# Kernel tuning notes

Measured on AMD Instinct MI355X. Metric: run time of the kernel, lower is better.

## Reference

```python
import jax, jax.numpy as jnp
import numpy as np

N_NODES = 100000
N_EDGES = 1600000
N_GRAPHS = 256
D = 128
L = 3
N_OUT = 10


def setup_inputs() -> dict:
    key = jax.random.key(0)
    ks = jax.random.split(key, 6)
    x = jax.random.normal(ks[0], (N_NODES, D), dtype=jnp.float32)
    edge_index = jax.random.randint(ks[1], (2, N_EDGES), 0, N_NODES, dtype=jnp.int64)
    batch = jnp.sort(jax.random.randint(ks[2], (N_NODES,), 0, N_GRAPHS, dtype=jnp.int64))
    conv_w = jax.random.normal(ks[3], (L, D, D), dtype=jnp.float32) * (1.0 / np.sqrt(D))
    conv_b = jnp.zeros((L, D), dtype=jnp.float32)
    out_w = jax.random.normal(ks[4], (3 * D, N_OUT), dtype=jnp.float32) * (1.0 / np.sqrt(3 * D))
    out_b = jnp.zeros((N_OUT,), dtype=jnp.float32)
    return {"x": x, "edge_index": edge_index, "batch": batch,
            "conv_w": conv_w, "conv_b": conv_b, "out_w": out_w, "out_b": out_b}


def reference(x, edge_index, batch, conv_w, conv_b, out_w, out_b):
    N = x.shape[0]
    # --- add self-loops (PyG GCNConv default) ---
    loop = jnp.arange(N, dtype=edge_index.dtype)
    src = jnp.concatenate([edge_index[0], loop])  # [E+N]
    dst = jnp.concatenate([edge_index[1], loop])
    # --- symmetric normalization: deg computed on dst (col) ---
    deg = jax.ops.segment_sum(jnp.ones_like(dst, dtype=x.dtype), dst, num_segments=N)
    dinv = jnp.where(deg > 0, jax.lax.rsqrt(jnp.maximum(deg, 1.0)), 0.0)
    norm = dinv[src] * dinv[dst]  # [E+N]

    h = x
    for l in range(conv_w.shape[0]):
        h = h @ conv_w[l]                                   # [N, D] transform first
        msg = h[src] * norm[:, None]                        # gather + scale
        h = jax.ops.segment_sum(msg, dst, num_segments=N)   # scatter-add
        h = jax.nn.relu(h + conv_b[l])

    # --- global max / mean / add pooling over graphs ---
    B = N_GRAPHS
    gmax = jax.ops.segment_max(h, batch, num_segments=B)
    gsum = jax.ops.segment_sum(h, batch, num_segments=B)
    cnt = jax.ops.segment_sum(jnp.ones((N, 1), h.dtype), batch, num_segments=B)
    gmean = gsum / jnp.maximum(cnt, 1.0)
    pooled = jnp.concatenate([gmax, gmean, gsum], axis=1)   # [B, 3D]
    # dropout p=0.5 is identity in eval mode
    return pooled @ out_w + out_b
```

## Files before the change

### kernel.cpp

```cpp
#include <hip/hip_runtime.h>
#include <hip/hip_bf16.h>

#define D 128
#define NP 8
#define DPB 64
#define KPB (DPB * NP)
#define SUB 64
#define CAP_SUB 64

typedef __attribute__((ext_vector_type(8))) __bf16 bf16x8;
typedef __attribute__((ext_vector_type(4))) float f32x4;
typedef __attribute__((ext_vector_type(4))) short s16x4;
typedef __attribute__((ext_vector_type(8))) short s16x8;

static __device__ __forceinline__ short f2bf(float f) {
    union { float f; unsigned u; } in; in.f = f;
    unsigned u = in.u;
    u += 0x7fffu + ((u >> 16) & 1u);
    return (short)(u >> 16);
}

__global__ void k_bucket(const int* __restrict__ src, const int* __restrict__ dst,
                         int* __restrict__ bcnt, int* __restrict__ staging,
                         int E, int KBE) {
    int i = blockIdx.x * 256 + threadIdx.x;
    if (i >= E) return;
    int d = dst[i], s = src[i];
    int b = d >> 6;
    int key = ((d & 63) << 3) | (s >> 14);
    int j = blockIdx.x & (SUB - 1);
    int slot = atomicAdd(&bcnt[j * KBE + b], 1);
    if (slot < CAP_SUB) staging[((size_t)j * KBE + b) * CAP_SUB + slot] = (key << 17) | s;
}

__global__ void k_btot(const int* __restrict__ bcnt, int* __restrict__ btot, int KBE) {
    int b = blockIdx.x * 256 + threadIdx.x;
    if (b >= KBE) return;
    int v = 0;
    #pragma unroll
    for (int j = 0; j < SUB; j++) {
        int c = bcnt[j * KBE + b];
        v += (c > CAP_SUB) ? CAP_SUB : c;
    }
    btot[b] = v;
}

__global__ void k_bscan(const int* __restrict__ btot, int* __restrict__ bbase,
                        int* __restrict__ row_ptr, int nkeys, int KBE) {
    __shared__ int sm[512];
    __shared__ int carry;
    int t = threadIdx.x;
    if (t == 0) carry = 0;
    __syncthreads();
    for (int c0 = 0; c0 < KBE; c0 += 512) {
        int b = c0 + t;
        int v = (b < KBE) ? btot[b] : 0;
        sm[t] = v;
        __syncthreads();
        for (int off = 1; off < 512; off <<= 1) {
            int x = (t >= off) ? sm[t - off] : 0;
            __syncthreads();
            sm[t] += x;
            __syncthreads();
        }
        if (b < KBE) bbase[b] = sm[t] - v + carry;
        __syncthreads();
        if (t == 0) carry += sm[511];
        __syncthreads();
    }
    if (t == 0) { bbase[KBE] = carry; row_ptr[nkeys] = carry; }
}

__global__ __launch_bounds__(256) void k_build(
    const int* __restrict__ staging, const int* __restrict__ bcnt,
    const int* __restrict__ bbase, int* __restrict__ row_ptr,
    int* __restrict__ csr_src, float* __restrict__ dinv, int N, int KBE)
{
    const int b = blockIdx.x;
    const int tid = threadIdx.x;
    __shared__ int cnt[KPB];
    __shared__ int subn[SUB];
    __shared__ int chunkbuf[256];
    __shared__ int carry;

    if (tid < SUB) {
        int c = bcnt[tid * KBE + b];
        subn[tid] = (c > CAP_SUB) ? CAP_SUB : c;
    }
    for (int k = tid; k < KPB; k += 256) cnt[k] = 0;
    if (tid == 0) carry = 0;
    __syncthreads();

    const int base = bbase[b];
    const int nb = bbase[b + 1] - base;
    const int j = tid >> 2, l4 = tid & 3;
    const int* __restrict__ sreg = staging + ((size_t)j * KBE + b) * CAP_SUB;
    const int sn = subn[j];

    for (int e = l4; e < sn; e += 4)
        atomicAdd(&cnt[sreg[e] >> 17], 1);
    __syncthreads();

    #pragma unroll 1
    for (int c = 0; c < KPB / 256; c++) {
        int idx = c * 256 + tid;
        int v = cnt[idx];
        chunkbuf[tid] = v;
        __syncthreads();
        for (int off = 1; off < 256; off <<= 1) {
            int x = (tid >= off) ? chunkbuf[tid - off] : 0;
            __syncthreads();
            chunkbuf[tid] += x;
            __syncthreads();
        }
        cnt[idx] = chunkbuf[tid] - v + carry;
        __syncthreads();
        if (tid == 255) carry += chunkbuf[255];
        __syncthreads();
    }

    for (int k = tid; k < KPB; k += 256)
        row_ptr[(size_t)b * KPB + k] = base + cnt[k];
    for (int dl = tid; dl < DPB; dl += 256) {
        int d = b * DPB + dl;
        if (d < N) {
            int hi2 = (dl == DPB - 1) ? nb : cnt[(dl + 1) * NP];
            int deg = hi2 - cnt[dl * NP];
            dinv[d] = rsqrtf((float)deg + 1.0f);
        }
    }
    __syncthreads();

    for (int e = l4; e < sn; e += 4) {
        int w = sreg[e];
        int slot = base + atomicAdd(&cnt[w >> 17], 1);
        csr_src[slot] = w & 0x1FFFF;
    }
}

__global__ void k_gseg(const int* __restrict__ batch, int* __restrict__ gstart,
                       int* __restrict__ gcnt, int N, int B) {
    int g = blockIdx.x * blockDim.x + threadIdx.x;
    if (g > B) return;
    int lo = 0, hi = N;
    while (lo < hi) {
        int mid = (lo + hi) >> 1;
        if (batch[mid] < g) lo = mid + 1; else hi = mid;
    }
    gstart[g] = lo;
    if (g < B) {
        int lo2 = lo, hi2 = N;
        while (lo2 < hi2) {
            int mid = (lo2 + hi2) >> 1;
            if (batch[mid] < g + 1) lo2 = mid + 1; else hi2 = mid;
        }
        gcnt[g] = lo2 - lo;
    }
}

__global__ void k_cvt_x(const float* __restrict__ x, const float* __restrict__ dinv,
                        short* __restrict__ xb, int total4) {
    int i = blockIdx.x * blockDim.x + threadIdx.x;
    if (i < total4) {
        float d = dinv[i >> 5];
        float4 v = ((const float4*)x)[i];
        s16x4 o;
        o.x = f2bf(v.x * d); o.y = f2bf(v.y * d);
        o.z = f2bf(v.z * d); o.w = f2bf(v.w * d);
        ((s16x4*)xb)[i] = o;
    }
}

__global__ void k_cvt_w(const float* __restrict__ W, short* __restrict__ Wt, int total) {
    int i = blockIdx.x * blockDim.x + threadIdx.x;
    if (i < total) {
        int l = i >> 14;
        int rem = i & 16383;
        int n = rem >> 7;
        int k = rem & 127;
        Wt[i] = f2bf(W[(l << 14) + (k << 7) + n]);
    }
}

__global__ __launch_bounds__(256) void k_layer(
    const short* __restrict__ hin, const int* __restrict__ row_ptr,
    const int* __restrict__ csr_src, const float* __restrict__ dinv,
    const short* __restrict__ Wt, const float* __restrict__ bias,
    short* __restrict__ hout, float* __restrict__ hrelu, int N, int mode)
{
    __shared__ __align__(16) short tile[16 * 128];
    const int tid = threadIdx.x;
    const int wave = tid >> 6;
    const int lane = tid & 63;
    const int group = lane >> 4;
    const int lg = lane & 15;
    const int off = lg * 8;
    const int node_base = blockIdx.x * 16;
    const int r = wave * 4 + group;
    const int i = node_base + r;

    short* dstp = &tile[r * 128 + ((lg ^ (r & 7)) << 3)];
    if (i < N) {
        float acc[8];
        bf16x8 v = *(const bf16x8*)(hin + (size_t)i * D + off);
        #pragma unroll
        for (int k = 0; k < 8; k++) acc[k] = (float)v[k];

        int t = row_ptr[i * NP];
        const int end = row_ptr[i * NP + NP];
        for (; t + 4 <= end; t += 4) {
            int i0 = csr_src[t + 0], i1 = csr_src[t + 1];
            int i2 = csr_src[t + 2], i3 = csr_src[t + 3];
            bf16x8 v0 = *(const bf16x8*)(hin + (size_t)i0 * D + off);
            bf16x8 v1 = *(const bf16x8*)(hin + (size_t)i1 * D + off);
            bf16x8 v2 = *(const bf16x8*)(hin + (size_t)i2 * D + off);
            bf16x8 v3 = *(const bf16x8*)(hin + (size_t)i3 * D + off);
            #pragma unroll
            for (int k = 0; k < 8; k++)
                acc[k] += (((float)v0[k] + (float)v1[k]) + ((float)v2[k] + (float)v3[k]));
        }
        for (; t < end; t++) {
            int i0 = csr_src[t];
            bf16x8 v0 = *(const bf16x8*)(hin + (size_t)i0 * D + off);
            #pragma unroll
            for (int k = 0; k < 8; k++) acc[k] += (float)v0[k];
        }

        const float di = dinv[i];
        s16x8 o;
        #pragma unroll
        for (int k = 0; k < 8; k++) o[k] = f2bf(acc[k] * di);
        *(s16x8*)dstp = o;
    } else {
        s16x8 z = {0, 0, 0, 0, 0, 0, 0, 0};
        *(s16x8*)dstp = z;
    }
    __syncthreads();

    bf16x8 afrag[4];
    #pragma unroll
    for (int kt = 0; kt < 4; kt++)
        afrag[kt] = *(const bf16x8*)(&tile[lg * 128 + (((group + 4 * kt) ^ (lg & 7)) << 3)]);

    f32x4 acc2[2];
    #pragma unroll
    for (int nt = 0; nt < 2; nt++) { f32x4 z = {0.f, 0.f, 0.f, 0.f}; acc2[nt] = z; }
    #pragma unroll
    for (int nt = 0; nt < 2; nt++) {
        const short* bp = Wt + (size_t)(wave * 32 + nt * 16 + lg) * D + group * 8;
        #pragma unroll
        for (int kt = 0; kt < 4; kt++) {
            bf16x8 b = *(const bf16x8*)(bp + kt * 32);
            acc2[nt] = __builtin_amdgcn_mfma_f32_16x16x32_bf16(afrag[kt], b, acc2[nt], 0, 0, 0);
        }
    }

    float bcol[2];
    #pragma unroll
    for (int nt = 0; nt < 2; nt++) bcol[nt] = bias[wave * 32 + nt * 16 + lg];
    const int row0 = node_base + group * 4;
    #pragma unroll
    for (int i2 = 0; i2 < 4; i2++) {
        int r2 = row0 + i2;
        if (r2 < N) {
            if (mode == 0) {
                float dr = dinv[r2];
                #pragma unroll
                for (int nt = 0; nt < 2; nt++) {
                    int col = wave * 32 + nt * 16 + lg;
                    float val = fmaxf(acc2[nt][i2] + bcol[nt], 0.0f);
                    hout[(size_t)r2 * D + col] = f2bf(val * dr);
                }
            } else {
                #pragma unroll
                for (int nt = 0; nt < 2; nt++) {
                    int col = wave * 32 + nt * 16 + lg;
                    hrelu[(size_t)r2 * D + col] = fmaxf(acc2[nt][i2] + bcol[nt], 0.0f);
                }
            }
        }
    }
}

__global__ __launch_bounds__(256) void k_pool(const float* __restrict__ hrelu,
                                              const int* __restrict__ gstart,
                                              const int* __restrict__ gcnt,
                                              float* __restrict__ pmax,
                                              float* __restrict__ psum, int B) {
    int g = blockIdx.x >> 2;
    int q = blockIdx.x & 3;
    int c = threadIdx.x & 127;
    int p = threadIdx.x >> 7;
    int start = gstart[g];
    int endr = start + gcnt[g];

    float mx0 = 0.f, mx1 = 0.f, sm0 = 0.f, sm1 = 0.f;
    int r = start + q * 2 + p;
    for (; r + 8 < endr; r += 16) {
        float v0 = hrelu[(size_t)r * D + c];
        float v1 = hrelu[(size_t)(r + 8) * D + c];
        mx0 = fmaxf(mx0, v0); sm0 += v0;
        mx1 = fmaxf(mx1, v1); sm1 += v1;
    }
    if (r < endr) {
        float v0 = hrelu[(size_t)r * D + c];
        mx0 = fmaxf(mx0, v0); sm0 += v0;
    }
    float mx = fmaxf(mx0, mx1), sm = sm0 + sm1;

    __shared__ float smx[128], ssm[128];
    if (p == 1) { smx[c] = mx; ssm[c] = sm; }
    __syncthreads();
    if (p == 0) {
        pmax[((size_t)q * B + g) * D + c] = fmaxf(mx, smx[c]);
        psum[((size_t)q * B + g) * D + c] = sm + ssm[c];
    }
}

__global__ void k_final(const float* __restrict__ pmax, const float* __restrict__ psum,
                        const int* __restrict__ gcnt, const float* __restrict__ ow,
                        const float* __restrict__ ob, float* __restrict__ out, int B) {
    int g = blockIdx.x;
    int t = threadIdx.x;
    float part[10];
    #pragma unroll
    for (int o = 0; o < 10; o++) part[o] = 0.f;
    float invc = 1.0f / fmaxf((float)gcnt[g], 1.0f);
    for (int k = t; k < 3 * D; k += 64) {
        int c = (k < D) ? k : ((k < 2 * D) ? k - D : k - 2 * D);
        float pk;
        if (k < D) {
            float m = pmax[(size_t)g * D + c];
            #pragma unroll
            for (int q = 1; q < 4; q++) m = fmaxf(m, pmax[((size_t)q * B + g) * D + c]);
            pk = m;
        } else {
            float s = psum[(size_t)g * D + c];
            #pragma unroll
            for (int q = 1; q < 4; q++) s += psum[((size_t)q * B + g) * D + c];
            pk = (k < 2 * D) ? s * invc : s;
        }
        const float* w = ow + k * 10;
        #pragma unroll
        for (int o = 0; o < 10; o++) part[o] += pk * w[o];
    }
    #pragma unroll
    for (int off = 32; off > 0; off >>= 1)
        #pragma unroll
        for (int o = 0; o < 10; o++) part[o] += __shfl_down(part[o], off, 64);
    if (t == 0)
        #pragma unroll
        for (int o = 0; o < 10; o++) out[g * 10 + o] = part[o] + ob[o];
}

extern "C" void kernel_launch(void* const* d_in, const int* in_sizes, int n_in,
                              void* d_out, int out_size, void* d_ws, size_t ws_size,
                              hipStream_t stream) {
    const float* x     = (const float*)d_in[0];
    const int*   ei    = (const int*)d_in[1];
    const int*   batch = (const int*)d_in[2];
    const float* convw = (const float*)d_in[3];
    const float* convb = (const float*)d_in[4];
    const float* outw  = (const float*)d_in[5];
    const float* outb  = (const float*)d_in[6];
    float* out = (float*)d_out;

    const int N = in_sizes[0] / D;
    const int E = in_sizes[1] / 2;
    const int L = in_sizes[3] / (D * D);
    const int B = out_size / 10;

    const int* src = ei;
    const int* dst = ei + E;

    const int KBE   = (N + DPB - 1) / DPB;
    const int nkeys = KBE * KPB;

    char* p = (char*)d_ws;
    auto alloc = [&](size_t bytes) { char* r = p; p += (bytes + 255) & ~255ull; return r; };
    short* hb0     = (short*)alloc((size_t)N * D * 2);
    short* hb1     = (short*)alloc((size_t)N * D * 2);
    float* hrelu   = (float*)alloc((size_t)N * D * 4);
    short* Wt      = (short*)alloc((size_t)L * D * D * 2);
    int*   row_ptr = (int*)alloc(((size_t)nkeys + 1) * 4);
    int*   csr_src = (int*)alloc((size_t)E * 4);
    int*   bcnt    = (int*)alloc((size_t)SUB * KBE * 4);
    int*   btot    = (int*)alloc((size_t)KBE * 4);
    int*   bbase   = (int*)alloc(((size_t)KBE + 1) * 4);
    float* dinv    = (float*)alloc((size_t)N * 4);
    float* pmax    = (float*)alloc((size_t)4 * B * D * 4);
    float* psum    = (float*)alloc((size_t)4 * B * D * 4);
    int*   gcnt    = (int*)alloc((size_t)B * 4);
    int*   gstart  = (int*)alloc(((size_t)B + 1) * 4);

    int* staging = (int*)hrelu;

    hipMemsetAsync(bcnt, 0, (size_t)SUB * KBE * 4, stream);

    k_bucket<<<(E + 255) / 256, 256, 0, stream>>>(src, dst, bcnt, staging, E, KBE);
    k_gseg<<<1, 512, 0, stream>>>(batch, gstart, gcnt, N, B);
    k_btot<<<(KBE + 255) / 256, 256, 0, stream>>>(bcnt, btot, KBE);
    k_bscan<<<1, 512, 0, stream>>>(btot, bbase, row_ptr, nkeys, KBE);
    k_build<<<KBE, 256, 0, stream>>>(staging, bcnt, bbase, row_ptr, csr_src, dinv, N, KBE);
    k_cvt_x<<<((N * D / 4) + 255) / 256, 256, 0, stream>>>(x, dinv, hb0, N * D / 4);
    k_cvt_w<<<((L * D * D) + 255) / 256, 256, 0, stream>>>(convw, Wt, L * D * D);

    const int lblocks = (N + 15) / 16;
    k_layer<<<lblocks, 256, 0, stream>>>(hb0, row_ptr, csr_src, dinv, Wt,
                                         convb, hb1, hrelu, N, 0);
    k_layer<<<lblocks, 256, 0, stream>>>(hb1, row_ptr, csr_src, dinv, Wt + D * D,
                                         convb + D, hb0, hrelu, N, 0);
    k_layer<<<lblocks, 256, 0, stream>>>(hb0, row_ptr, csr_src, dinv, Wt + 2 * D * D,
                                         convb + 2 * D, hb1, hrelu, N, 1);

    k_pool<<<B * 4, 256, 0, stream>>>(hrelu, gstart, gcnt, pmax, psum, B);
    k_final<<<B, 64, 0, stream>>>(pmax, psum, gcnt, outw, outb, out, B);
}
```

Baseline: 461.0 us.

## Make each wave own 16 nodes end-to-end and drop block-wide barrier

Restructures the fused layer kernel so each wave aggregates 16 nodes (four rounds of four) into its own LDS tile, then computes all 128 output columns for those nodes with MFMA. The block-level __syncthreads is replaced by a wave-local LDS waitcnt, so waves no longer stall on each other's gathers. Blocks now cover 64 nodes, and the neighbor gather is unrolled by 8 to keep more loads in flight. In exchange, each wave reads the full weight matrix instead of a quarter of it, uses more accumulator registers, and LDS per block grows fourfold.

New measurement: 483.0 us. +4.8%, slower.

```diff
diff --git a/kernel.cpp b/kernel.cpp
--- a/kernel.cpp
+++ b/kernel.cpp
@@ -188,77 +188,101 @@
     const short* __restrict__ Wt, const float* __restrict__ bias,
     short* __restrict__ hout, float* __restrict__ hrelu, int N, int mode)
 {
-    __shared__ __align__(16) short tile[16 * 128];
+    __shared__ __align__(16) short tile[4][16 * 128];
     const int tid = threadIdx.x;
     const int wave = tid >> 6;
     const int lane = tid & 63;
     const int group = lane >> 4;
     const int lg = lane & 15;
     const int off = lg * 8;
-    const int node_base = blockIdx.x * 16;
-    const int r = wave * 4 + group;
-    const int i = node_base + r;
-
-    short* dstp = &tile[r * 128 + ((lg ^ (r & 7)) << 3)];
-    if (i < N) {
-        float acc[8];
-        bf16x8 v = *(const bf16x8*)(hin + (size_t)i * D + off);
-        #pragma unroll
-        for (int k = 0; k < 8; k++) acc[k] = (float)v[k];
-
-        int t = row_ptr[i * NP];
-        const int end = row_ptr[i * NP + NP];
-        for (; t + 4 <= end; t += 4) {
-            int i0 = csr_src[t + 0], i1 = csr_src[t + 1];
-            int i2 = csr_src[t + 2], i3 = csr_src[t + 3];
-            bf16x8 v0 = *(const bf16x8*)(hin + (size_t)i0 * D + off);
-            bf16x8 v1 = *(const bf16x8*)(hin + (size_t)i1 * D + off);
-            bf16x8 v2 = *(const bf16x8*)(hin + (size_t)i2 * D + off);
-            bf16x8 v3 = *(const bf16x8*)(hin + (size_t)i3 * D + off);
+    const int wbase = blockIdx.x * 64 + wave * 16;
+    short* wtile = &tile[wave][0];
+
+    #pragma unroll 1
+    for (int rd = 0; rd < 4; rd++) {
+        const int r = rd * 4 + group;
+        const int i = wbase + r;
+        short* dstp = &wtile[r * 128 + ((lg ^ (r & 7)) << 3)];
+        if (i < N) {
+            float acc[8];
+            bf16x8 v = *(const bf16x8*)(hin + (size_t)i * D + off);
             #pragma unroll
-            for (int k = 0; k < 8; k++)
-                acc[k] += (((float)v0[k] + (float)v1[k]) + ((float)v2[k] + (float)v3[k]));
-        }
-        for (; t < end; t++) {
-            int i0 = csr_src[t];
-            bf16x8 v0 = *(const bf16x8*)(hin + (size_t)i0 * D + off);
+            for (int k = 0; k < 8; k++) acc[k] = (float)v[k];
+
+            int t = row_ptr[i * NP];
+            const int end = row_ptr[i * NP + NP];
+            for (; t + 8 <= end; t += 8) {
+                int i0 = csr_src[t + 0], i1 = csr_src[t + 1];
+                int i2 = csr_src[t + 2], i3 = csr_src[t + 3];
+                int i4 = csr_src[t + 4], i5 = csr_src[t + 5];
+                int i6 = csr_src[t + 6], i7 = csr_src[t + 7];
+                bf16x8 v0 = *(const bf16x8*)(hin + (size_t)i0 * D + off);
+                bf16x8 v1 = *(const bf16x8*)(hin + (size_t)i1 * D + off);
+                bf16x8 v2 = *(const bf16x8*)(hin + (size_t)i2 * D + off);
+                bf16x8 v3 = *(const bf16x8*)(hin + (size_t)i3 * D + off);
+                bf16x8 v4 = *(const bf16x8*)(hin + (size_t)i4 * D + off);
+                bf16x8 v5 = *(const bf16x8*)(hin + (size_t)i5 * D + off);
+                bf16x8 v6 = *(const bf16x8*)(hin + (size_t)i6 * D + off);
+                bf16x8 v7 = *(const bf16x8*)(hin + (size_t)i7 * D + off);
+                #pragma unroll
+                for (int k = 0; k < 8; k++)
+                    acc[k] += ((((float)v0[k] + (float)v1[k]) + ((float)v2[k] + (float)v3[k]))
+                             + (((float)v4[k] + (float)v5[k]) + ((float)v6[k] + (float)v7[k])));
+            }
+            for (; t + 4 <= end; t += 4) {
+                int i0 = csr_src[t + 0], i1 = csr_src[t + 1];
+                int i2 = csr_src[t + 2], i3 = csr_src[t + 3];
+                bf16x8 v0 = *(const bf16x8*)(hin + (size_t)i0 * D + off);
+                bf16x8 v1 = *(const bf16x8*)(hin + (size_t)i1 * D + off);
+                bf16x8 v2 = *(const bf16x8*)(hin + (size_t)i2 * D + off);
+                bf16x8 v3 = *(const bf16x8*)(hin + (size_t)i3 * D + off);
+                #pragma unroll
+                for (int k = 0; k < 8; k++)
+                    acc[k] += (((float)v0[k] + (float)v1[k]) + ((float)v2[k] + (float)v3[k]));
+            }
+            for (; t < end; t++) {
+                int i0 = csr_src[t];
+                bf16x8 v0 = *(const bf16x8*)(hin + (size_t)i0 * D + off);
+                #pragma unroll
+                for (int k = 0; k < 8; k++) acc[k] += (float)v0[k];
+            }
+
+            const float di = dinv[i];
+            s16x8 o;
             #pragma unroll
-            for (int k = 0; k < 8; k++) acc[k] += (float)v0[k];
-        }
-
-        const float di = dinv[i];
-        s16x8 o;
-        #pragma unroll
-        for (int k = 0; k < 8; k++) o[k] = f2bf(acc[k] * di);
-        *(s16x8*)dstp = o;
-    } else {
-        s16x8 z = {0, 0, 0, 0, 0, 0, 0, 0};
-        *(s16x8*)dstp = z;
-    }
-    __syncthreads();
+            for (int k = 0; k < 8; k++) o[k] = f2bf(acc[k] * di);
+            *(s16x8*)dstp = o;
+        } else {
+            s16x8 z = {0, 0, 0, 0, 0, 0, 0, 0};
+            *(s16x8*)dstp = z;
+        }
+    }
+
+    __asm__ volatile("s_waitcnt lgkmcnt(0)" ::: "memory");
+    __builtin_amdgcn_sched_barrier(0);
 
     bf16x8 afrag[4];
     #pragma unroll
     for (int kt = 0; kt < 4; kt++)
-        afrag[kt] = *(const bf16x8*)(&tile[lg * 128 + (((group + 4 * kt) ^ (lg & 7)) << 3)]);
-
-    f32x4 acc2[2];
-    #pragma unroll
-    for (int nt = 0; nt < 2; nt++) { f32x4 z = {0.f, 0.f, 0.f, 0.f}; acc2[nt] = z; }
-    #pragma unroll
-    for (int nt = 0; nt < 2; nt++) {
-        const short* bp = Wt + (size_t)(wave * 32 + nt * 16 + lg) * D + group * 8;
+        afrag[kt] = *(const bf16x8*)(&wtile[lg * 128 + (((group + 4 * kt) ^ (lg & 7)) << 3)]);
+
+    f32x4 acc2[8];
+    #pragma unroll
+    for (int ct = 0; ct < 8; ct++) { f32x4 z = {0.f, 0.f, 0.f, 0.f}; acc2[ct] = z; }
+    #pragma unroll
+    for (int ct = 0; ct < 8; ct++) {
+        const short* bp = Wt + (size_t)(ct * 16 + lg) * D + group * 8;
         #pragma unroll
         for (int kt = 0; kt < 4; kt++) {
             bf16x8 b = *(const bf16x8*)(bp + kt * 32);
-            acc2[nt] = __builtin_amdgcn_mfma_f32_16x16x32_bf16(afrag[kt], b, acc2[nt], 0, 0, 0);
-        }
-    }
-
-    float bcol[2];
-    #pragma unroll
-    for (int nt = 0; nt < 2; nt++) bcol[nt] = bias[wave * 32 + nt * 16 + lg];
-    const int row0 = node_base + group * 4;
+            acc2[ct] = __builtin_amdgcn_mfma_f32_16x16x32_bf16(afrag[kt], b, acc2[ct], 0, 0, 0);
+        }
+    }
+
+    float bcol[8];
+    #pragma unroll
+    for (int ct = 0; ct < 8; ct++) bcol[ct] = bias[ct * 16 + lg];
+    const int row0 = wbase + group * 4;
     #pragma unroll
     for (int i2 = 0; i2 < 4; i2++) {
         int r2 = row0 + i2;
@@ -266,16 +290,16 @@
             if (mode == 0) {
                 float dr = dinv[r2];
                 #pragma unroll
-                for (int nt = 0; nt < 2; nt++) {
-                    int col = wave * 32 + nt * 16 + lg;
-                    float val = fmaxf(acc2[nt][i2] + bcol[nt], 0.0f);
+                for (int ct = 0; ct < 8; ct++) {
+                    int col = ct * 16 + lg;
+                    float val = fmaxf(acc2[ct][i2] + bcol[ct], 0.0f);
                     hout[(size_t)r2 * D + col] = f2bf(val * dr);
                 }
             } else {
                 #pragma unroll
-                for (int nt = 0; nt < 2; nt++) {
-                    int col = wave * 32 + nt * 16 + lg;
-                    hrelu[(size_t)r2 * D + col] = fmaxf(acc2[nt][i2] + bcol[nt], 0.0f);
+                for (int ct = 0; ct < 8; ct++) {
+                    int col = ct * 16 + lg;
+                    hrelu[(size_t)r2 * D + col] = fmaxf(acc2[ct][i2] + bcol[ct], 0.0f);
                 }
             }
         }
@@ -405,7 +429,7 @@
     k_cvt_x<<<((N * D / 4) + 255) / 256, 256, 0, stream>>>(x, dinv, hb0, N * D / 4);
     k_cvt_w<<<((L * D * D) + 255) / 256, 256, 0, stream>>>(convw, Wt, L * D * D);
 
-    const int lblocks = (N + 15) / 16;
+    const int lblocks = (N + 63) / 64;
     k_layer<<<lblocks, 256, 0, stream>>>(hb0, row_ptr, csr_src, dinv, Wt,
                                          convb, hb1, hrelu, N, 0);
     k_layer<<<lblocks, 256, 0, stream>>>(hb1, row_ptr, csr_src, dinv, Wt + D * D,
```

## Reorder nodes by in-degree so layer blocks process similar-degree nodes

Applied to the files above, without the earlier changes.

Adds a counting sort of nodes by clamped in-degree: k_build records each node's degree and a per-subgroup histogram, k_dscan scans it, and k_dscat writes a permutation. The layer kernels then take node indices through this permutation, so the 16 rows in a block have similar gather loop lengths. This is meant to reduce wave divergence and load imbalance in the neighbor aggregation. The cost is two extra small kernels, an extra memset, and scattered reads and writes of node rows, which loses the spatial locality of processing consecutive nodes.

After: 476.9 us. 3.4% more time.

```diff
diff --git a/kernel.cpp b/kernel.cpp
--- a/kernel.cpp
+++ b/kernel.cpp
@@ -7,6 +7,7 @@
 #define KPB (DPB * NP)
 #define SUB 64
 #define CAP_SUB 64
+#define DSUB 64
 
 typedef __attribute__((ext_vector_type(8))) __bf16 bf16x8;
 typedef __attribute__((ext_vector_type(4))) float f32x4;
@@ -74,7 +75,8 @@
 __global__ __launch_bounds__(256) void k_build(
     const int* __restrict__ staging, const int* __restrict__ bcnt,
     const int* __restrict__ bbase, int* __restrict__ row_ptr,
-    int* __restrict__ csr_src, float* __restrict__ dinv, int N, int KBE)
+    int* __restrict__ csr_src, float* __restrict__ dinv,
+    int* __restrict__ deg_arr, int* __restrict__ dsub, int N, int KBE)
 {
     const int b = blockIdx.x;
     const int tid = threadIdx.x;
@@ -127,6 +129,9 @@
             int hi2 = (dl == DPB - 1) ? nb : cnt[(dl + 1) * NP];
             int deg = hi2 - cnt[dl * NP];
             dinv[d] = rsqrtf((float)deg + 1.0f);
+            int dc = (deg > 255) ? 255 : deg;
+            deg_arr[d] = dc;
+            atomicAdd(&dsub[((b & (DSUB - 1)) << 8) + dc], 1);
         }
     }
     __syncthreads();
@@ -136,6 +141,36 @@
         int slot = base + atomicAdd(&cnt[w >> 17], 1);
         csr_src[slot] = w & 0x1FFFF;
     }
+}
+
+__global__ void k_dscan(const int* __restrict__ dsub, int* __restrict__ dcur) {
+    __shared__ int sm[256];
+    const int d = threadIdx.x;
+    int tot = 0;
+    for (int jj = 0; jj < DSUB; jj++) tot += dsub[(jj << 8) + d];
+    sm[d] = tot;
+    __syncthreads();
+    for (int off = 1; off < 256; off <<= 1) {
+        int x = (d >= off) ? sm[d - off] : 0;
+        __syncthreads();
+        sm[d] += x;
+        __syncthreads();
+    }
+    int run = sm[d] - tot;
+    for (int jj = 0; jj < DSUB; jj++) {
+        dcur[(jj << 8) + d] = run;
+        run += dsub[(jj << 8) + d];
+    }
+}
+
+__global__ void k_dscat(const int* __restrict__ deg_arr, int* __restrict__ dcur,
+                        int* __restrict__ perm, int N) {
+    int i = blockIdx.x * 256 + threadIdx.x;
+    if (i >= N) return;
+    int dc = deg_arr[i];
+    int jj = (i >> 6) & (DSUB - 1);
+    int pos = atomicAdd(&dcur[(jj << 8) + dc], 1);
+    perm[pos] = i;
 }
 
 __global__ void k_gseg(const int* __restrict__ batch, int* __restrict__ gstart,
@@ -185,6 +220,7 @@
 __global__ __launch_bounds__(256) void k_layer(
     const short* __restrict__ hin, const int* __restrict__ row_ptr,
     const int* __restrict__ csr_src, const float* __restrict__ dinv,
+    const int* __restrict__ perm,
     const short* __restrict__ Wt, const float* __restrict__ bias,
     short* __restrict__ hout, float* __restrict__ hrelu, int N, int mode)
 {
@@ -197,10 +233,11 @@
     const int off = lg * 8;
     const int node_base = blockIdx.x * 16;
     const int r = wave * 4 + group;
-    const int i = node_base + r;
+    const int ti = node_base + r;
 
     short* dstp = &tile[r * 128 + ((lg ^ (r & 7)) << 3)];
-    if (i < N) {
+    if (ti < N) {
+        const int i = perm[ti];
         float acc[8];
         bf16x8 v = *(const bf16x8*)(hin + (size_t)i * D + off);
         #pragma unroll
@@ -263,19 +300,20 @@
     for (int i2 = 0; i2 < 4; i2++) {
         int r2 = row0 + i2;
         if (r2 < N) {
+            const int n2 = perm[r2];
             if (mode == 0) {
-                float dr = dinv[r2];
+                float dr = dinv[n2];
                 #pragma unroll
                 for (int nt = 0; nt < 2; nt++) {
                     int col = wave * 32 + nt * 16 + lg;
                     float val = fmaxf(acc2[nt][i2] + bcol[nt], 0.0f);
-                    hout[(size_t)r2 * D + col] = f2bf(val * dr);
+                    hout[(size_t)n2 * D + col] = f2bf(val * dr);
                 }
             } else {
                 #pragma unroll
                 for (int nt = 0; nt < 2; nt++) {
                     int col = wave * 32 + nt * 16 + lg;
-                    hrelu[(size_t)r2 * D + col] = fmaxf(acc2[nt][i2] + bcol[nt], 0.0f);
+                    hrelu[(size_t)n2 * D + col] = fmaxf(acc2[nt][i2] + bcol[nt], 0.0f);
                 }
             }
         }
@@ -392,25 +430,33 @@
     float* psum    = (float*)alloc((size_t)4 * B * D * 4);
     int*   gcnt    = (int*)alloc((size_t)B * 4);
     int*   gstart  = (int*)alloc(((size_t)B + 1) * 4);
+    int*   deg_arr = (int*)alloc((size_t)N * 4);
+    int*   dsub    = (int*)alloc((size_t)DSUB * 256 * 4);
+    int*   dcur    = (int*)alloc((size_t)DSUB * 256 * 4);
+    int*   perm    = (int*)alloc((size_t)N * 4);
 
     int* staging = (int*)hrelu;
 
     hipMemsetAsync(bcnt, 0, (size_t)SUB * KBE * 4, stream);
+    hipMemsetAsync(dsub, 0, (size_t)DSUB * 256 * 4, stream);
 
     k_bucket<<<(E + 255) / 256, 256, 0, stream>>>(src, dst, bcnt, staging, E, KBE);
     k_gseg<<<1, 512, 0, stream>>>(batch, gstart, gcnt, N, B);
     k_btot<<<(KBE + 255) / 256, 256, 0, stream>>>(bcnt, btot, KBE);
     k_bscan<<<1, 512, 0, stream>>>(btot, bbase, row_ptr, nkeys, KBE);
-    k_build<<<KBE, 256, 0, stream>>>(staging, bcnt, bbase, row_ptr, csr_src, dinv, N, KBE);
+    k_build<<<KBE, 256, 0, stream>>>(staging, bcnt, bbase, row_ptr, csr_src, dinv,
+                                     deg_arr, dsub, N, KBE);
+    k_dscan<<<1, 256, 0, stream>>>(dsub, dcur);
+    k_dscat<<<(N + 255) / 256, 256, 0, stream>>>(deg_arr, dcur, perm, N);
     k_cvt_x<<<((N * D / 4) + 255) / 256, 256, 0, stream>>>(x, dinv, hb0, N * D / 4);
     k_cvt_w<<<((L * D * D) + 255) / 256, 256, 0, stream>>>(convw, Wt, L * D * D);
 
     const int lblocks = (N + 15) / 16;
-    k_layer<<<lblocks, 256, 0, stream>>>(hb0, row_ptr, csr_src, dinv, Wt,
+    k_layer<<<lblocks, 256, 0, stream>>>(hb0, row_ptr, csr_src, dinv, perm, Wt,
                                          convb, hb1, hrelu, N, 0);
-    k_layer<<<lblocks, 256, 0, stream>>>(hb1, row_ptr, csr_src, dinv, Wt + D * D,
+    k_layer<<<lblocks, 256, 0, stream>>>(hb1, row_ptr, csr_src, dinv, perm, Wt + D * D,
                                          convb + D, hb0, hrelu, N, 0);
-    k_layer<<<lblocks, 256, 0, stream>>>(hb0, row_ptr, csr_src, dinv, Wt + 2 * D * D,
+    k_layer<<<lblocks, 256, 0, stream>>>(hb0, row_ptr, csr_src, dinv, perm, Wt + 2 * D * D,
                                          convb + 2 * D, hb1, hrelu, N, 1);
 
     k_pool<<<B * 4, 256, 0, stream>>>(hrelu, gstart, gcnt, pmax, psum, B);
```

## Process 128 nodes per block with source-partitioned interleaved gather and larger MFMA tile

Applied to the files above, without the earlier changes.

Each layer block now handles 128 nodes instead of 16. Each 16-lane group gathers neighbours for 8 nodes at once, walking 16 source-index partitions in lockstep so that concurrent gathers touch nearby rows of the input, which is meant to improve L2 locality. The row pointers are staged in shared memory. Each wave then runs a 32x128 MFMA tile, so weight loads are amortised over more rows. The costs are much higher register pressure from 64 float accumulators per lane, a launch bound of 3 blocks per CU, divergence across nodes with uneven degree, and fewer blocks overall.

After: 1.159 ms. +151.4%, slower.

```diff
diff --git a/kernel.cpp b/kernel.cpp
--- a/kernel.cpp
+++ b/kernel.cpp
@@ -2,11 +2,13 @@
 #include <hip/hip_bf16.h>
 
 #define D 128
-#define NP 8
+#define NP 16
 #define DPB 64
 #define KPB (DPB * NP)
 #define SUB 64
 #define CAP_SUB 64
+#define NPG 8
+#define NBLK 128
 
 typedef __attribute__((ext_vector_type(8))) __bf16 bf16x8;
 typedef __attribute__((ext_vector_type(4))) float f32x4;
@@ -27,7 +29,7 @@
     if (i >= E) return;
     int d = dst[i], s = src[i];
     int b = d >> 6;
-    int key = ((d & 63) << 3) | (s >> 14);
+    int key = ((d & 63) << 4) | (s >> 13);
     int j = blockIdx.x & (SUB - 1);
     int slot = atomicAdd(&bcnt[j * KBE + b], 1);
     if (slot < CAP_SUB) staging[((size_t)j * KBE + b) * CAP_SUB + slot] = (key << 17) | s;
@@ -182,100 +184,144 @@
     }
 }
 
-__global__ __launch_bounds__(256) void k_layer(
+__global__ __launch_bounds__(256, 3) void k_layer(
     const short* __restrict__ hin, const int* __restrict__ row_ptr,
     const int* __restrict__ csr_src, const float* __restrict__ dinv,
     const short* __restrict__ Wt, const float* __restrict__ bias,
-    short* __restrict__ hout, float* __restrict__ hrelu, int N, int mode)
+    short* __restrict__ hout, float* __restrict__ hrelu, int N, int nkeys, int mode)
 {
-    __shared__ __align__(16) short tile[16 * 128];
+    __shared__ __align__(16) short tile[NBLK * 128];
+    __shared__ int rp[NBLK * NP + 1];
     const int tid = threadIdx.x;
     const int wave = tid >> 6;
     const int lane = tid & 63;
     const int group = lane >> 4;
+    const int gidx = wave * 4 + group;
     const int lg = lane & 15;
     const int off = lg * 8;
-    const int node_base = blockIdx.x * 16;
-    const int r = wave * 4 + group;
-    const int i = node_base + r;
-
-    short* dstp = &tile[r * 128 + ((lg ^ (r & 7)) << 3)];
-    if (i < N) {
-        float acc[8];
-        bf16x8 v = *(const bf16x8*)(hin + (size_t)i * D + off);
-        #pragma unroll
-        for (int k = 0; k < 8; k++) acc[k] = (float)v[k];
-
-        int t = row_ptr[i * NP];
-        const int end = row_ptr[i * NP + NP];
-        for (; t + 4 <= end; t += 4) {
-            int i0 = csr_src[t + 0], i1 = csr_src[t + 1];
-            int i2 = csr_src[t + 2], i3 = csr_src[t + 3];
-            bf16x8 v0 = *(const bf16x8*)(hin + (size_t)i0 * D + off);
-            bf16x8 v1 = *(const bf16x8*)(hin + (size_t)i1 * D + off);
-            bf16x8 v2 = *(const bf16x8*)(hin + (size_t)i2 * D + off);
-            bf16x8 v3 = *(const bf16x8*)(hin + (size_t)i3 * D + off);
-            #pragma unroll
-            for (int k = 0; k < 8; k++)
-                acc[k] += (((float)v0[k] + (float)v1[k]) + ((float)v2[k] + (float)v3[k]));
-        }
-        for (; t < end; t++) {
-            int i0 = csr_src[t];
-            bf16x8 v0 = *(const bf16x8*)(hin + (size_t)i0 * D + off);
-            #pragma unroll
-            for (int k = 0; k < 8; k++) acc[k] += (float)v0[k];
-        }
-
-        const float di = dinv[i];
+    const int node_base = blockIdx.x * NBLK;
+
+    {
+        const int base_k = node_base * NP;
+        for (int k = tid; k < NBLK * NP + 1; k += 256) {
+            int gi = base_k + k;
+            rp[k] = row_ptr[(gi <= nkeys) ? gi : nkeys];
+        }
+    }
+    __syncthreads();
+
+    const int ln0 = gidx * NPG;
+    float acc[NPG][8];
+    #pragma unroll
+    for (int n = 0; n < NPG; n++) {
+        int i = node_base + ln0 + n;
+        if (i < N) {
+            bf16x8 v = *(const bf16x8*)(hin + (size_t)i * D + off);
+            #pragma unroll
+            for (int k = 0; k < 8; k++) acc[n][k] = (float)v[k];
+        } else {
+            #pragma unroll
+            for (int k = 0; k < 8; k++) acc[n][k] = 0.f;
+        }
+    }
+
+    #pragma unroll 1
+    for (int s = 0; s < NP; s++) {
+        int ts[NPG], es[NPG];
+        #pragma unroll
+        for (int n = 0; n < NPG; n++) {
+            ts[n] = rp[(ln0 + n) * NP + s];
+            es[n] = rp[(ln0 + n) * NP + s + 1];
+        }
+        for (;;) {
+            bool a[NPG];
+            bool any = false;
+            #pragma unroll
+            for (int n = 0; n < NPG; n++) { a[n] = ts[n] < es[n]; any |= a[n]; }
+            if (!__any((int)any)) break;
+            int idx[NPG];
+            #pragma unroll
+            for (int n = 0; n < NPG; n++) if (a[n]) idx[n] = csr_src[ts[n]];
+            bf16x8 v[NPG];
+            #pragma unroll
+            for (int n = 0; n < NPG; n++) if (a[n])
+                v[n] = *(const bf16x8*)(hin + (size_t)idx[n] * D + off);
+            #pragma unroll
+            for (int n = 0; n < NPG; n++) if (a[n]) {
+                #pragma unroll
+                for (int k = 0; k < 8; k++) acc[n][k] += (float)v[n][k];
+                ts[n]++;
+            }
+        }
+    }
+
+    #pragma unroll
+    for (int n = 0; n < NPG; n++) {
+        const int ln = ln0 + n;
+        const int i = node_base + ln;
         s16x8 o;
-        #pragma unroll
-        for (int k = 0; k < 8; k++) o[k] = f2bf(acc[k] * di);
-        *(s16x8*)dstp = o;
-    } else {
-        s16x8 z = {0, 0, 0, 0, 0, 0, 0, 0};
-        *(s16x8*)dstp = z;
-    }
-    __syncthreads();
-
-    bf16x8 afrag[4];
-    #pragma unroll
-    for (int kt = 0; kt < 4; kt++)
-        afrag[kt] = *(const bf16x8*)(&tile[lg * 128 + (((group + 4 * kt) ^ (lg & 7)) << 3)]);
-
-    f32x4 acc2[2];
-    #pragma unroll
-    for (int nt = 0; nt < 2; nt++) { f32x4 z = {0.f, 0.f, 0.f, 0.f}; acc2[nt] = z; }
-    #pragma unroll
-    for (int nt = 0; nt < 2; nt++) {
-        const short* bp = Wt + (size_t)(wave * 32 + nt * 16 + lg) * D + group * 8;
+        if (i < N) {
+            const float di = dinv[i];
+            #pragma unroll
+            for (int k = 0; k < 8; k++) o[k] = f2bf(acc[n][k] * di);
+        } else {
+            #pragma unroll
+            for (int k = 0; k < 8; k++) o[k] = 0;
+        }
+        *(s16x8*)(&tile[ln * 128 + ((lg ^ (ln & 7)) << 3)]) = o;
+    }
+    __syncthreads();
+
+    bf16x8 aa[2][4];
+    #pragma unroll
+    for (int rt = 0; rt < 2; rt++)
+        #pragma unroll
+        for (int kt = 0; kt < 4; kt++) {
+            const int R = wave * 32 + rt * 16 + lg;
+            aa[rt][kt] = *(const bf16x8*)(&tile[R * 128 + (((group + 4 * kt) ^ (R & 7)) << 3)]);
+        }
+
+    f32x4 c2[2][8];
+    #pragma unroll
+    for (int rt = 0; rt < 2; rt++)
+        #pragma unroll
+        for (int ct = 0; ct < 8; ct++) { f32x4 z = {0.f, 0.f, 0.f, 0.f}; c2[rt][ct] = z; }
+
+    #pragma unroll
+    for (int ct = 0; ct < 8; ct++) {
+        const short* bp = Wt + (size_t)(ct * 16 + lg) * D + group * 8;
         #pragma unroll
         for (int kt = 0; kt < 4; kt++) {
             bf16x8 b = *(const bf16x8*)(bp + kt * 32);
-            acc2[nt] = __builtin_amdgcn_mfma_f32_16x16x32_bf16(afrag[kt], b, acc2[nt], 0, 0, 0);
-        }
-    }
-
-    float bcol[2];
-    #pragma unroll
-    for (int nt = 0; nt < 2; nt++) bcol[nt] = bias[wave * 32 + nt * 16 + lg];
-    const int row0 = node_base + group * 4;
-    #pragma unroll
-    for (int i2 = 0; i2 < 4; i2++) {
-        int r2 = row0 + i2;
-        if (r2 < N) {
-            if (mode == 0) {
-                float dr = dinv[r2];
-                #pragma unroll
-                for (int nt = 0; nt < 2; nt++) {
-                    int col = wave * 32 + nt * 16 + lg;
-                    float val = fmaxf(acc2[nt][i2] + bcol[nt], 0.0f);
-                    hout[(size_t)r2 * D + col] = f2bf(val * dr);
-                }
-            } else {
-                #pragma unroll
-                for (int nt = 0; nt < 2; nt++) {
-                    int col = wave * 32 + nt * 16 + lg;
-                    hrelu[(size_t)r2 * D + col] = fmaxf(acc2[nt][i2] + bcol[nt], 0.0f);
+            #pragma unroll
+            for (int rt = 0; rt < 2; rt++)
+                c2[rt][ct] = __builtin_amdgcn_mfma_f32_16x16x32_bf16(aa[rt][kt], b, c2[rt][ct], 0, 0, 0);
+        }
+    }
+
+    float bcol[8];
+    #pragma unroll
+    for (int ct = 0; ct < 8; ct++) bcol[ct] = bias[ct * 16 + lg];
+    #pragma unroll
+    for (int rt = 0; rt < 2; rt++) {
+        const int row0 = node_base + wave * 32 + rt * 16 + group * 4;
+        #pragma unroll
+        for (int i2 = 0; i2 < 4; i2++) {
+            const int r2 = row0 + i2;
+            if (r2 < N) {
+                if (mode == 0) {
+                    const float dr = dinv[r2];
+                    #pragma unroll
+                    for (int ct = 0; ct < 8; ct++) {
+                        float val = fmaxf(c2[rt][ct][i2] + bcol[ct], 0.0f);
+                        hout[(size_t)r2 * D + ct * 16 + lg] = f2bf(val * dr);
+                    }
+                } else {
+                    #pragma unroll
+                    for (int ct = 0; ct < 8; ct++) {
+                        hrelu[(size_t)r2 * D + ct * 16 + lg] =
+                            fmaxf(c2[rt][ct][i2] + bcol[ct], 0.0f);
+                    }
                 }
             }
         }
@@ -405,13 +451,13 @@
     k_cvt_x<<<((N * D / 4) + 255) / 256, 256, 0, stream>>>(x, dinv, hb0, N * D / 4);
     k_cvt_w<<<((L * D * D) + 255) / 256, 256, 0, stream>>>(convw, Wt, L * D * D);
 
-    const int lblocks = (N + 15) / 16;
+    const int lblocks = (N + NBLK - 1) / NBLK;
     k_layer<<<lblocks, 256, 0, stream>>>(hb0, row_ptr, csr_src, dinv, Wt,
-                                         convb, hb1, hrelu, N, 0);
+                                         convb, hb1, hrelu, N, nkeys, 0);
     k_layer<<<lblocks, 256, 0, stream>>>(hb1, row_ptr, csr_src, dinv, Wt + D * D,
-                                         convb + D, hb0, hrelu, N, 0);
+                                         convb + D, hb0, hrelu, N, nkeys, 0);
     k_layer<<<lblocks, 256, 0, stream>>>(hb0, row_ptr, csr_src, dinv, Wt + 2 * D * D,
-                                         convb + 2 * D, hb1, hrelu, N, 1);
+                                         convb + 2 * D, hb1, hrelu, N, nkeys, 1);
 
     k_pool<<<B * 4, 256, 0, stream>>>(hrelu, gstart, gcnt, pmax, psum, B);
     k_final<<<B, 64, 0, stream>>>(pmax, psum, gcnt, outw, outb, out, B);
```
